# Performance work log

Hardware: AMD Instinct MI355X
Metric: run time of the kernel (lower is better)

## Reference

```python
import jax, jax.numpy as jnp
import numpy as np

B, LQ, LD, H, DIM, PF = 16, 64, 2048, 1024, 128, 4
MAXK = LD // PF + 1  # static upper bound on num clusters (valid_len <= LD)


def setup_inputs() -> dict:
    key = jax.random.key(0)
    k1, k2, k3, k4 = jax.random.split(key, 4)
    return {
        "q_hidden": jax.random.normal(k1, (B, LQ, H), jnp.float32),
        "d_hidden": jax.random.normal(k2, (B, LD, H), jnp.float32),
        "W": jax.random.normal(k3, (H, DIM), jnp.float32) * (1.0 / np.sqrt(H)),  # xavier-ish
        "b": jnp.zeros((DIM,), jnp.float32),
        "q_mask": jnp.ones((B, LQ), jnp.int32),
        "d_mask": jnp.ones((B, LD), jnp.int32),
        "labels": jax.random.randint(k4, (B, LD), 0, MAXK, dtype=jnp.int32),
        "pooling_factor": PF,
    }


def _encode(hidden, W, b, mask):
    # proj -> L2 normalize -> zero out padded tokens
    r = hidden @ W + b
    r = r / jnp.clip(jnp.linalg.norm(r, axis=-1, keepdims=True), 1e-12)
    return r * mask[..., None].astype(r.dtype)


def _pool(d_repr, d_mask, labels, pf):
    # segment-mean per batch sample, cluster labels supplied externally
    Bn, L, D = d_repr.shape
    max_k = L // pf + 1  # static
    valid = jnp.clip(d_mask.sum(-1), 2, None)          # [B]
    k = valid // pf + 1                                 # per-sample num clusters
    lab = jnp.where(d_mask > 0, labels % k[:, None], max_k)  # invalid tokens -> dummy seg
    seg = lambda vals, idx: jax.ops.segment_sum(vals, idx, num_segments=max_k + 1)
    sums = jax.vmap(seg)(d_repr, lab)[:, :max_k]                          # [B,K,D]
    counts = jax.vmap(seg)(jnp.where(d_mask > 0, 1.0, 0.0), lab)[:, :max_k]
    means = sums / jnp.clip(counts, 1.0)[..., None]
    means = means / jnp.clip(jnp.linalg.norm(means, axis=-1, keepdims=True), 1e-12)
    pad_mask = jnp.arange(max_k)[None, :] < k[:, None]                    # [B,K]
    return means * pad_mask[..., None], pad_mask


def reference(q_hidden, d_hidden, W, b, q_mask, d_mask, labels, pooling_factor):
    q = _encode(q_hidden, W, b, q_mask)            # [B,LQ,DIM]
    d = _encode(d_hidden, W, b, d_mask)            # [B,LD,DIM]
    d_pool, pmask = _pool(d, d_mask, labels, pooling_factor)  # [B,K,DIM]
    sim = jnp.einsum('bqd,bkd->bqk', q, d_pool)
    sim = jnp.where(pmask[:, None, :], sim, -1e4)
    score = (sim.max(-1) * q_mask.astype(sim.dtype)).sum(-1)  # maxsum per pair
    return score
```

## Files before the change

### kernel.cpp

```cpp
#include <hip/hip_runtime.h>
#include <hip/hip_bf16.h>

#define BB    16
#define LQ    64
#define LD    2048
#define HH    1024
#define DIM   128
#define MAXK  513
#define SCH   9

typedef __attribute__((ext_vector_type(8))) short short8;
typedef __attribute__((ext_vector_type(4))) float f32x4;

__device__ __forceinline__ float b2f(ushort u) {
    union { float f; unsigned int u32; } c; c.u32 = ((unsigned int)u) << 16; return c.f;
}
__device__ __forceinline__ ushort f2b_rn(float f) {
    unsigned int x = __float_as_uint(f);
    return (ushort)((x + 0x7fffu + ((x >> 16) & 1u)) >> 16);
}

__device__ __forceinline__ void gld16(void* lds, const void* g) {
    __builtin_amdgcn_global_load_lds(
        (const __attribute__((address_space(1))) unsigned int*)g,
        (__attribute__((address_space(3))) unsigned int*)lds,
        16, 0, 0);
}

__global__ __launch_bounds__(256) void prep_kb_kernel(
    const float* __restrict__ W,
    const int*   __restrict__ d_mask,
    const int*   __restrict__ pf,
    ushort*      __restrict__ Wt,
    int*         __restrict__ kvals,
    float*       __restrict__ sums)
{
    int bid = blockIdx.x, t = threadIdx.x;
    if (bid < 16) {
        __shared__ ushort tile[128][72];
        const int h0 = bid * 64;
        #pragma unroll
        for (int i = 0; i < 32; ++i) {
            int flat = i * 256 + t;
            int r = flat >> 7, c = flat & 127;
            tile[c][r] = f2b_rn(W[(long)(h0 + r) * DIM + c]);
        }
        __syncthreads();
        #pragma unroll
        for (int i = 0; i < 4; ++i) {
            int flat = i * 256 + t;
            int n = flat >> 3, u = flat & 7;
            uint4 v = *(const uint4*)&tile[n][u * 8];
            *(uint4*)&Wt[(long)n * HH + h0 + u * 8] = v;
        }
    } else if (bid < 32) {
        __shared__ int red[4];
        int b = bid - 16;
        int lane = t & 63, wave = t >> 6;
        int s = 0;
        for (int i = t; i < LD; i += 256) s += (d_mask[b * LD + i] > 0) ? 1 : 0;
        #pragma unroll
        for (int m = 1; m < 64; m <<= 1) s += __shfl_xor(s, m);
        if (lane == 0) red[wave] = s;
        __syncthreads();
        if (t == 0) {
            int v = red[0] + red[1] + red[2] + red[3];
            if (v < 2) v = 2;
            int pfv = pf[0];
            if (pfv < 1 || pfv > LD) pfv = 4;
            kvals[b] = v / pfv + 1;
        }
    } else {
        const int total4 = (BB * MAXK * DIM) / 4;
        float4* s4 = (float4*)sums;
        const float4 z = make_float4(0.f, 0.f, 0.f, 0.f);
        for (int i = (bid - 32) * 256 + t; i < total4; i += 256 * 256)
            s4[i] = z;
    }
}

__global__ __launch_bounds__(512, 4) void encode_kernel(
    const float*  __restrict__ X,
    const ushort* __restrict__ Wt,
    const float*  __restrict__ bias,
    const int*    __restrict__ mask,
    const int*    __restrict__ labels,
    const int*    __restrict__ kvals,
    float*        __restrict__ sums,
    float*        __restrict__ q_repr,
    int           isq)
{
    __shared__ __align__(16) uint4 Wlds[4096];

    const int t = threadIdx.x;
    const int w = t >> 6, lane = t & 63;
    const int m16 = lane & 15, quad = lane >> 4;

    const int unit = blockIdx.x * 8 + w;
    const long row0 = (long)unit * 16;
    const float* aptr = X + (row0 + m16) * HH + quad * 8;

    f32x4 acc[8];
    #pragma unroll
    for (int j = 0; j < 8; ++j) acc[j] = (f32x4){0.f, 0.f, 0.f, 0.f};

    const int sw8 = m16 & 7;
    const ushort* Wu = (const ushort*)Wlds;

    float4 ast[4][2];
    ast[0][0] = *(const float4*)(aptr);
    ast[0][1] = *(const float4*)(aptr + 4);
    ast[1][0] = *(const float4*)(aptr + 32);
    ast[1][1] = *(const float4*)(aptr + 36);
    ast[2][0] = *(const float4*)(aptr + 64);
    ast[2][1] = *(const float4*)(aptr + 68);

    #pragma unroll
    for (int p = 0; p < 4; ++p) {
        __syncthreads();
        #pragma unroll
        for (int i = 0; i < 8; ++i) {
            int Si = w * 512 + i * 64 + lane;
            int n = Si >> 5, up = Si & 31;
            const ushort* src = Wt + (long)n * HH + (p * 32 + (up ^ (n & 7))) * 8;
            gld16(&Wlds[w * 512 + i * 64], src);
        }
        __syncthreads();
        #pragma unroll
        for (int cc = 0; cc < 8; ++cc) {
            const int c = p * 8 + cc;
            if (c + 3 < 32) {
                ast[(c + 3) & 3][0] = *(const float4*)(aptr + (c + 3) * 32);
                ast[(c + 3) & 3][1] = *(const float4*)(aptr + (c + 3) * 32 + 4);
            }
            float av[8];
            *(float4*)(av)     = ast[c & 3][0];
            *(float4*)(av + 4) = ast[c & 3][1];
            short8 ah;
            #pragma unroll
            for (int j = 0; j < 8; ++j) ah[j] = (short)f2b_rn(av[j]);
            #pragma unroll
            for (int ct = 0; ct < 8; ++ct) {
                short8 bf = *(const short8*)
                    &Wu[(ct * 16 + m16) * 256 + ((cc * 4 + quad) ^ sw8) * 8];
                acc[ct] = __builtin_amdgcn_mfma_f32_16x16x32_bf16(ah, bf, acc[ct], 0, 0, 0);
            }
        }
    }

    float bia[8];
    #pragma unroll
    for (int ct = 0; ct < 8; ++ct) bia[ct] = bias[ct * 16 + m16];

    float vv[8][4];
    float ssp[4] = {0.f, 0.f, 0.f, 0.f};
    #pragma unroll
    for (int ct = 0; ct < 8; ++ct)
        #pragma unroll
        for (int r = 0; r < 4; ++r) {
            vv[ct][r] = acc[ct][r] + bia[ct];
            ssp[r] += vv[ct][r] * vv[ct][r];
        }
    #pragma unroll
    for (int r = 0; r < 4; ++r) {
        ssp[r] += __shfl_xor(ssp[r], 1);
        ssp[r] += __shfl_xor(ssp[r], 2);
        ssp[r] += __shfl_xor(ssp[r], 4);
        ssp[r] += __shfl_xor(ssp[r], 8);
    }

    #pragma unroll
    for (int r = 0; r < 4; ++r) {
        long rowg = row0 + quad * 4 + r;
        float scale = 1.0f / fmaxf(sqrtf(ssp[r]), 1e-12f);
        if (isq) {
            scale *= (float)mask[rowg];
            #pragma unroll
            for (int ct = 0; ct < 8; ++ct)
                q_repr[rowg * DIM + ct * 16 + m16] = vv[ct][r] * scale;
        } else if (mask[rowg] > 0) {
            int b = (int)(rowg >> 11);
            int seg = labels[rowg] % kvals[b];
            float* sp = sums + ((long)b * MAXK + seg) * DIM + m16;
            #pragma unroll
            for (int ct = 0; ct < 8; ++ct)
                atomicAdd(sp + ct * 16, vv[ct][r] * scale);
        }
    }
}

__global__ __launch_bounds__(256) void simmax_kernel(
    const float* __restrict__ q_repr,
    const float* __restrict__ sums,
    const int*   __restrict__ kvals,
    float*       __restrict__ pmax)
{
    __shared__ __align__(16) ushort Qh[64 * 136];
    __shared__ __align__(16) ushort Ql[64 * 136];
    __shared__ __align__(16) ushort Ch[64 * 136];
    __shared__ float cn[64];

    int b = blockIdx.x / SCH, chunk = blockIdx.x % SCH;
    int t = threadIdx.x, w = t >> 6, lane = t & 63;
    int m16 = lane & 15, quad = lane >> 4;

    #pragma unroll
    for (int i = 0; i < 8; ++i) {
        int flat = i * 256 + t;
        int row = flat >> 5, c4 = flat & 31;
        float4 v = *(const float4*)(q_repr + ((long)b * LQ + row) * DIM + c4 * 4);
        float x[4]; *(float4*)x = v;
        ushort4 h, l;
        ushort* hp = (ushort*)&h; ushort* lp = (ushort*)&l;
        #pragma unroll
        for (int j = 0; j < 4; ++j) {
            unsigned int ux = __float_as_uint(x[j]);
            hp[j] = (ushort)(ux >> 16);
            lp[j] = f2b_rn(x[j] - __uint_as_float(ux & 0xffff0000u));
        }
        *(ushort4*)&Qh[row * 136 + c4 * 4] = h;
        *(ushort4*)&Ql[row * 136 + c4 * 4] = l;
    }
    #pragma unroll
    for (int i = 0; i < 8; ++i) {
        int flat = i * 256 + t;
        int row = flat >> 5, c4 = flat & 31;
        int kk = chunk * 64 + row;
        float4 v = (kk < MAXK)
            ? *(const float4*)(sums + ((long)b * MAXK + kk) * DIM + c4 * 4)
            : make_float4(0.f, 0.f, 0.f, 0.f);
        ushort4 h; ushort* hp = (ushort*)&h;
        hp[0] = f2b_rn(v.x); hp[1] = f2b_rn(v.y);
        hp[2] = f2b_rn(v.z); hp[3] = f2b_rn(v.w);
        *(ushort4*)&Ch[row * 136 + c4 * 4] = h;
    }
    __syncthreads();

    {
        int c = w * 16 + m16;
        float ssv = 0.f;
        #pragma unroll
        for (int j = 0; j < 16; ++j) {
            unsigned int u = *(const unsigned int*)&Ch[c * 136 + quad * 32 + j * 2];
            float x0 = b2f((ushort)u), x1 = b2f((ushort)(u >> 16));
            ssv += x0 * x0 + x1 * x1;
        }
        ssv += __shfl_xor(ssv, 16);
        ssv += __shfl_xor(ssv, 32);
        if (quad == 0) cn[c] = (ssv > 1e-24f) ? rsqrtf(ssv) : 0.f;
    }
    __syncthreads();

    f32x4 acc[4];
    #pragma unroll
    for (int j = 0; j < 4; ++j) acc[j] = (f32x4){0.f, 0.f, 0.f, 0.f};

    #pragma unroll
    for (int kc = 0; kc < 4; ++kc) {
        short8 qh = *(const short8*)&Qh[(w * 16 + m16) * 136 + kc * 32 + quad * 8];
        short8 ql = *(const short8*)&Ql[(w * 16 + m16) * 136 + kc * 32 + quad * 8];
        #pragma unroll
        for (int ct = 0; ct < 4; ++ct) {
            short8 cf = *(const short8*)&Ch[(ct * 16 + m16) * 136 + kc * 32 + quad * 8];
            acc[ct] = __builtin_amdgcn_mfma_f32_16x16x32_bf16(qh, cf, acc[ct], 0, 0, 0);
            acc[ct] = __builtin_amdgcn_mfma_f32_16x16x32_bf16(ql, cf, acc[ct], 0, 0, 0);
        }
    }

    int kb = kvals[b];
    #pragma unroll
    for (int r = 0; r < 4; ++r) {
        float mx = -1e4f;
        #pragma unroll
        for (int ct = 0; ct < 4; ++ct) {
            int cl = chunk * 64 + ct * 16 + m16;
            float sim = acc[ct][r] * cn[ct * 16 + m16];
            mx = fmaxf(mx, (cl < kb) ? sim : -1e4f);
        }
        mx = fmaxf(mx, __shfl_xor(mx, 1));
        mx = fmaxf(mx, __shfl_xor(mx, 2));
        mx = fmaxf(mx, __shfl_xor(mx, 4));
        mx = fmaxf(mx, __shfl_xor(mx, 8));
        if (m16 == 0)
            pmax[((long)b * SCH + chunk) * 64 + w * 16 + quad * 4 + r] = mx;
    }
}

__global__ __launch_bounds__(64) void final_kernel(
    const float* __restrict__ pmax,
    const int*   __restrict__ q_mask,
    float*       __restrict__ out)
{
    int b = blockIdx.x, r = threadIdx.x;
    float m = -3e38f;
    #pragma unroll
    for (int c = 0; c < SCH; ++c)
        m = fmaxf(m, pmax[((long)b * SCH + c) * 64 + r]);
    m *= (float)q_mask[b * LQ + r];
    #pragma unroll
    for (int sh = 1; sh < 64; sh <<= 1) m += __shfl_xor(m, sh);
    if (r == 0) out[b] = m;
}

extern "C" void kernel_launch(void* const* d_in, const int* in_sizes, int n_in,
                              void* d_out, int out_size, void* d_ws, size_t ws_size,
                              hipStream_t stream) {
    const float* q_hidden = (const float*)d_in[0];
    const float* d_hidden = (const float*)d_in[1];
    const float* W        = (const float*)d_in[2];
    const float* bias     = (const float*)d_in[3];
    const int*   q_mask   = (const int*)d_in[4];
    const int*   d_mask   = (const int*)d_in[5];
    const int*   labels   = (const int*)d_in[6];
    const int*   pf       = (const int*)d_in[7];

    float* ws     = (float*)d_ws;
    float* q_repr = ws;
    float* sums   = q_repr + (long)BB * LQ * DIM;
    float* pmaxb  = sums + (long)BB * MAXK * DIM;
    int*   kvals  = (int*)(pmaxb + BB * SCH * 64);
    ushort* Wt    = (ushort*)(kvals + 16);

    prep_kb_kernel<<<288, 256, 0, stream>>>(W, d_mask, pf, Wt, kvals, sums);
    encode_kernel<<<8, 512, 0, stream>>>(q_hidden, Wt, bias, q_mask,
                                         labels, kvals, sums, q_repr, 1);
    encode_kernel<<<256, 512, 0, stream>>>(d_hidden, Wt, bias, d_mask,
                                           labels, kvals, sums, q_repr, 0);
    simmax_kernel<<<BB * SCH, 256, 0, stream>>>(q_repr, sums, kvals, pmaxb);
    final_kernel<<<BB, 64, 0, stream>>>(pmaxb, q_mask, (float*)d_out);
}
```

Measured before the change: 280.3 us.

## Stage activation tiles through LDS via async loads with smaller blocks

```diff
diff --git a/kernel.cpp b/kernel.cpp
--- a/kernel.cpp
+++ b/kernel.cpp
@@ -79,7 +79,7 @@
     }
 }
 
-__global__ __launch_bounds__(512, 4) void encode_kernel(
+__global__ __launch_bounds__(256, 2) void encode_kernel(
     const float*  __restrict__ X,
     const ushort* __restrict__ Wt,
     const float*  __restrict__ bias,
@@ -90,59 +90,58 @@
     float*        __restrict__ q_repr,
     int           isq)
 {
-    __shared__ __align__(16) uint4 Wlds[4096];
+    __shared__ __align__(16) uint4 lds[4096];
 
     const int t = threadIdx.x;
     const int w = t >> 6, lane = t & 63;
     const int m16 = lane & 15, quad = lane >> 4;
 
-    const int unit = blockIdx.x * 8 + w;
+    const int unit = blockIdx.x * 4 + w;
     const long row0 = (long)unit * 16;
-    const float* aptr = X + (row0 + m16) * HH + quad * 8;
 
     f32x4 acc[8];
     #pragma unroll
     for (int j = 0; j < 8; ++j) acc[j] = (f32x4){0.f, 0.f, 0.f, 0.f};
 
     const int sw8 = m16 & 7;
-    const ushort* Wu = (const ushort*)Wlds;
-
-    float4 ast[4][2];
-    ast[0][0] = *(const float4*)(aptr);
-    ast[0][1] = *(const float4*)(aptr + 4);
-    ast[1][0] = *(const float4*)(aptr + 32);
-    ast[1][1] = *(const float4*)(aptr + 36);
-    ast[2][0] = *(const float4*)(aptr + 64);
-    ast[2][1] = *(const float4*)(aptr + 68);
-
-    #pragma unroll
-    for (int p = 0; p < 4; ++p) {
+    const ushort* Wu = (const ushort*)lds;
+    const float4* Af = (const float4*)lds;
+    const int Abase = 2048 + w * 512;
+
+    const float* gA = X + (row0 + (lane >> 3)) * HH
+                        + (((lane & 7) ^ ((lane >> 3) & 7)) * 4);
+
+    #pragma unroll
+    for (int p = 0; p < 8; ++p) {
         __syncthreads();
         #pragma unroll
         for (int i = 0; i < 8; ++i) {
             int Si = w * 512 + i * 64 + lane;
-            int n = Si >> 5, up = Si & 31;
-            const ushort* src = Wt + (long)n * HH + (p * 32 + (up ^ (n & 7))) * 8;
-            gld16(&Wlds[w * 512 + i * 64], src);
+            int n = Si >> 4, up = Si & 15;
+            const ushort* src = Wt + (long)n * HH + (p * 16 + (up ^ (n & 7))) * 8;
+            gld16(&lds[w * 512 + i * 64], src);
+        }
+        #pragma unroll
+        for (int s = 0; s < 4; ++s) {
+            const long ko = (long)(p * 4 + s) * 32;
+            gld16(&lds[Abase + s * 128], gA + ko);
+            gld16(&lds[Abase + s * 128 + 64], gA + 8 * HH + ko);
         }
         __syncthreads();
         #pragma unroll
-        for (int cc = 0; cc < 8; ++cc) {
-            const int c = p * 8 + cc;
-            if (c + 3 < 32) {
-                ast[(c + 3) & 3][0] = *(const float4*)(aptr + (c + 3) * 32);
-                ast[(c + 3) & 3][1] = *(const float4*)(aptr + (c + 3) * 32 + 4);
-            }
+        for (int cc = 0; cc < 4; ++cc) {
+            float4 va0 = Af[Abase + cc * 128 + m16 * 8 + ((2 * quad) ^ sw8)];
+            float4 va1 = Af[Abase + cc * 128 + m16 * 8 + ((2 * quad + 1) ^ sw8)];
             float av[8];
-            *(float4*)(av)     = ast[c & 3][0];
-            *(float4*)(av + 4) = ast[c & 3][1];
+            *(float4*)(av)     = va0;
+            *(float4*)(av + 4) = va1;
             short8 ah;
             #pragma unroll
             for (int j = 0; j < 8; ++j) ah[j] = (short)f2b_rn(av[j]);
             #pragma unroll
             for (int ct = 0; ct < 8; ++ct) {
                 short8 bf = *(const short8*)
-                    &Wu[(ct * 16 + m16) * 256 + ((cc * 4 + quad) ^ sw8) * 8];
+                    &Wu[(ct * 16 + m16) * 128 + (((cc * 4 + quad)) ^ sw8) * 8];
                 acc[ct] = __builtin_amdgcn_mfma_f32_16x16x32_bf16(ah, bf, acc[ct], 0, 0, 0);
             }
         }
@@ -322,9 +321,9 @@
     ushort* Wt    = (ushort*)(kvals + 16);
 
     prep_kb_kernel<<<288, 256, 0, stream>>>(W, d_mask, pf, Wt, kvals, sums);
-    encode_kernel<<<8, 512, 0, stream>>>(q_hidden, Wt, bias, q_mask,
-                                         labels, kvals, sums, q_repr, 1);
-    encode_kernel<<<256, 512, 0, stream>>>(d_hidden, Wt, bias, d_mask,
+    encode_kernel<<<16, 256, 0, stream>>>(q_hidden, Wt, bias, q_mask,
+                                          labels, kvals, sums, q_repr, 1);
+    encode_kernel<<<512, 256, 0, stream>>>(d_hidden, Wt, bias, d_mask,
                                            labels, kvals, sums, q_repr, 0);
     simmax_kernel<<<BB * SCH, 256, 0, stream>>>(q_repr, sums, kvals, pmaxb);
     final_kernel<<<BB, 64, 0, stream>>>(pmaxb, q_mask, (float*)d_out);
```

Measured after the change: 255.9 us. 8.7% less time.
